# Optimization experiments

Measured on AMD Instinct MI355X. Metric: run time of the kernel, lower is better.

Reference implementation:

```python
import jax, jax.numpy as jnp
import numpy as np
from jax import lax

NUM_NODES = 100000
FEAT = 256
RANK = 16
NNZ = 4000000
NUM_HE = 125000  # num_hyperedges == num_edges_total
K = 2000000      # int(0.5 * NNZ)


def setup_inputs() -> dict:
    key = jax.random.key(0)
    ks = jax.random.split(key, 6)
    x = jax.random.normal(ks[0], (NUM_NODES, FEAT), dtype=jnp.float32)
    W = jax.random.normal(ks[1], (RANK, FEAT), dtype=jnp.float32)
    edge_factors = jax.random.normal(ks[2], (NUM_HE, RANK), dtype=jnp.float32)
    V_idx = jax.random.randint(ks[3], (NNZ,), 0, NUM_NODES, dtype=jnp.int32)
    E_idx = jax.random.randint(ks[4], (NNZ,), 0, NUM_HE, dtype=jnp.int32)
    edge_ids = jax.random.randint(ks[5], (NUM_HE,), 0, NUM_HE, dtype=jnp.int32)
    return {"x": x, "W": W, "edge_factors": edge_factors,
            "V_idx": V_idx, "E_idx": E_idx, "edge_ids": edge_ids, "k": K}


def _segment_mean(vals, seg_ids, num_segments):
    s = jax.ops.segment_sum(vals, seg_ids, num_segments=num_segments)
    c = jax.ops.segment_sum(jnp.ones_like(vals), seg_ids, num_segments=num_segments)
    return s / jnp.maximum(c, 1.0)


def reference(x, W, edge_factors, V_idx, E_idx, edge_ids, k):
    # node_proj(x): [N, rank]; gather per-incidence node and edge factors, dot product
    proj = x @ W.T                                  # [N, rank]
    ef = edge_factors[edge_ids[E_idx]]              # [nnz, rank]
    logits = jnp.sum(proj[V_idx] * ef, axis=-1)     # [nnz]
    scores = jax.nn.sigmoid(logits)

    # is_test=True path: deterministic top-k keep set
    _, keep_ids = lax.top_k(scores, k)
    hard = jnp.zeros_like(scores).at[keep_ids].set(1.0)
    # straight-through: forward == hard, gradient flows through scores where hard==1
    soft = hard + (scores - lax.stop_gradient(scores)) * hard

    edge_probs = _segment_mean(lax.stop_gradient(scores), E_idx, NUM_HE)
    edge_soft = _segment_mean(soft, E_idx, NUM_HE)
    edge_hard = (_segment_mean(hard, E_idx, NUM_HE) > 0).astype(jnp.float32)
    return scores, soft, hard, edge_probs, edge_soft, edge_hard
```

## Files before the change

kernel.cpp:

```cpp
#include <hip/hip_runtime.h>
#include <math.h>

#define FEAT 256
#define RANKK 16
#define CAND_CAP 131072
#define TIE_CAP 2048
#define NBK_MAX 512
#define PB_CHUNK 8192
#define SPLIT 4
#define PRJ_NODES 64
#define EH_BLOCKS 128
#define NW_BLOCKS 1024

typedef unsigned long long u64;

static __device__ __forceinline__ u64 pack_pair(unsigned e_low, unsigned bits, unsigned idx) {
    return ((u64)e_low << 56) | ((u64)bits << 26) | (u64)idx;
}
static __device__ __forceinline__ u64 pack_v(unsigned v, unsigned idx, unsigned e_low) {
    return ((u64)v << 40) | ((u64)idx << 8) | (u64)e_low;
}

__global__ __launch_bounds__(256) void prep_all(
        const int* __restrict__ E_idx, unsigned* __restrict__ bucketCnt,
        unsigned* __restrict__ bucketBase, unsigned* __restrict__ cursor,
        unsigned* __restrict__ ticket, int nnz,
        const float4* __restrict__ ef, const int* __restrict__ edge_ids,
        float4* __restrict__ ef2, int nhe,
        const float* __restrict__ x, const float* __restrict__ Wm,
        float* __restrict__ proj, int n_nodes, int G) {
    __shared__ float smem[12608];
    __shared__ unsigned isLast;
    int t = threadIdx.x;
    int bid = blockIdx.x;

    if (bid < EH_BLOCKS) {
        unsigned* h  = (unsigned*)smem;
        unsigned* ps = ((unsigned*)smem) + 512;
        for (int j = t; j < NBK_MAX; j += 256) h[j] = 0;
        __syncthreads();
        for (int i = bid * 256 + t; i < nnz; i += EH_BLOCKS * 256)
            atomicAdd(&h[((unsigned)E_idx[i]) >> 8], 1u);
        __syncthreads();
        for (int j = t; j < NBK_MAX; j += 256)
            if (h[j]) atomicAdd(&bucketCnt[j], h[j]);
        __threadfence();
        if (t == 0) isLast = (atomicAdd(ticket, 1u) == EH_BLOCKS - 1) ? 1u : 0u;
        __syncthreads();
        if (!isLast) return;
        unsigned a0 = atomicAdd(&bucketCnt[2 * t], 0u);
        unsigned a1 = atomicAdd(&bucketCnt[2 * t + 1], 0u);
        unsigned pairsum = a0 + a1;
        ps[t] = pairsum;
        __syncthreads();
        for (int off = 1; off < 256; off <<= 1) {
            unsigned v = (t >= off) ? ps[t - off] : 0u;
            __syncthreads();
            ps[t] += v;
            __syncthreads();
        }
        unsigned excl = ps[t] - pairsum;
        bucketBase[2 * t] = excl;           cursor[2 * t] = excl;
        bucketBase[2 * t + 1] = excl + a0;  cursor[2 * t + 1] = excl + a0;
        if (t == 255) bucketBase[NBK_MAX] = ps[255];
        return;
    }
    if (bid < EH_BLOCKS + G) {
        int tt = (bid - EH_BLOCKS) * 256 + t;
        if (tt < nhe * 4) {
            int e = tt >> 2, c = tt & 3;
            ef2[(size_t)e * 4 + c] = ef[(size_t)edge_ids[e] * 4 + c];
        }
        return;
    }
    int pb = bid - EH_BLOCKS - G;
    float (*Ws)[FEAT + 4] = (float(*)[FEAT + 4])smem;
    float (*Xs)[128 + 4]  = (float(*)[128 + 4])(smem + 4160);
    const float4* x4 = (const float4*)x;
    const float4* w4 = (const float4*)Wm;
    for (int i = t; i < RANKK * 64; i += 256) {
        int r = i >> 6, c4 = i & 63;
        *(float4*)&Ws[r][c4 * 4] = w4[(size_t)r * 64 + c4];
    }
    int nodeBase = pb * PRJ_NODES;
    int np = t >> 3, rp = t & 7;
    int n0 = np * 2, r0 = rp * 2;
    double a00 = 0.0, a01 = 0.0, a10 = 0.0, a11 = 0.0;
    for (int chunk = 0; chunk < 2; ++chunk) {
        __syncthreads();
        for (int i = t; i < PRJ_NODES * 32; i += 256) {
            int row = i >> 5, c4 = i & 31;
            int node = nodeBase + row;
            float4 v = make_float4(0.f, 0.f, 0.f, 0.f);
            if (node < n_nodes) v = x4[(size_t)node * 64 + chunk * 32 + c4];
            *(float4*)&Xs[row][c4 * 4] = v;
        }
        __syncthreads();
        int jw = chunk * 128;
        #pragma unroll 8
        for (int j4 = 0; j4 < 32; ++j4) {
            float4 xa = *(const float4*)&Xs[n0][j4 * 4];
            float4 xb = *(const float4*)&Xs[n0 + 1][j4 * 4];
            float4 wa = *(const float4*)&Ws[r0][jw + j4 * 4];
            float4 wb = *(const float4*)&Ws[r0 + 1][jw + j4 * 4];
            a00 += (double)xa.x * wa.x + (double)xa.y * wa.y + (double)xa.z * wa.z + (double)xa.w * wa.w;
            a01 += (double)xa.x * wb.x + (double)xa.y * wb.y + (double)xa.z * wb.z + (double)xa.w * wb.w;
            a10 += (double)xb.x * wa.x + (double)xb.y * wa.y + (double)xb.z * wa.z + (double)xb.w * wa.w;
            a11 += (double)xb.x * wb.x + (double)xb.y * wb.y + (double)xb.z * wb.z + (double)xb.w * wb.w;
        }
    }
    int nodeA = nodeBase + n0;
    int nodeB = nodeA + 1;
    if (nodeA < n_nodes) {
        proj[(size_t)nodeA * RANKK + r0]     = (float)a00;
        proj[(size_t)nodeA * RANKK + r0 + 1] = (float)a01;
    }
    if (nodeB < n_nodes) {
        proj[(size_t)nodeB * RANKK + r0]     = (float)a10;
        proj[(size_t)nodeB * RANKK + r0 + 1] = (float)a11;
    }
}

__global__ __launch_bounds__(256) void sort_kernel(const int* __restrict__ V_idx,
        const int* __restrict__ E_idx, u64* __restrict__ vlist,
        unsigned* __restrict__ cursor, int nnz, int nb) {
    __shared__ unsigned bh[NBK_MAX];
    int t = threadIdx.x;
    for (int j = t; j < NBK_MAX; j += 256) bh[j] = 0;
    __syncthreads();
    int base = blockIdx.x * PB_CHUNK;
    int nE = nnz - base;
    if (nE > PB_CHUNK) nE = PB_CHUNK;
    for (int o = t; o < nE; o += 256)
        atomicAdd(&bh[((unsigned)E_idx[base + o]) >> 8], 1u);
    __syncthreads();
    for (int b = t; b < nb; b += 256) {
        unsigned c = bh[b];
        bh[b] = c ? atomicAdd(&cursor[b], c) : 0u;
    }
    __syncthreads();
    for (int o = t; o < nE; o += 256) {
        int i = base + o;
        unsigned e = (unsigned)E_idx[i];
        unsigned v = (unsigned)V_idx[i];
        unsigned pos = atomicAdd(&bh[e >> 8], 1u);
        vlist[pos] = pack_v(v, (unsigned)i, e & 255u);
    }
}

__global__ __launch_bounds__(256) void bucket_score(
        const float4* __restrict__ proj4, const float4* __restrict__ ef4,
        const unsigned* __restrict__ bucketBase, u64* __restrict__ list,
        float* __restrict__ scores, int nhe) {
    __shared__ float efs[256][20];
    int t = threadIdx.x;
    int b = blockIdx.x >> 2;
    int part = blockIdx.x & (SPLIT - 1);
    for (int jj = t; jj < 1024; jj += 256) {
        int edge = (b << 8) + (jj >> 2);
        if (edge < nhe) {
            float4 v = ef4[(size_t)edge * 4 + (jj & 3)];
            *(float4*)&efs[jj >> 2][(jj & 3) * 4] = v;
        }
    }
    __syncthreads();
    unsigned n0 = bucketBase[b], n1 = bucketBase[b + 1];
    #pragma unroll 2
    for (unsigned j = n0 + (part << 8) + t; j < n1; j += SPLIT * 256) {
        u64 p = list[j];
        unsigned v   = (unsigned)(p >> 40);
        unsigned idx = (unsigned)(p >> 8) & 0xFFFFFFu;
        unsigned el  = (unsigned)(p & 255u);
        float4 p0 = proj4[(size_t)v * 4 + 0];
        float4 p1 = proj4[(size_t)v * 4 + 1];
        float4 p2 = proj4[(size_t)v * 4 + 2];
        float4 p3 = proj4[(size_t)v * 4 + 3];
        float4 f0 = *(const float4*)&efs[el][0];
        float4 f1 = *(const float4*)&efs[el][4];
        float4 f2 = *(const float4*)&efs[el][8];
        float4 f3 = *(const float4*)&efs[el][12];
        double acc = (double)p0.x * f0.x + (double)p0.y * f0.y + (double)p0.z * f0.z + (double)p0.w * f0.w
                   + (double)p1.x * f1.x + (double)p1.y * f1.y + (double)p1.z * f1.z + (double)p1.w * f1.w
                   + (double)p2.x * f2.x + (double)p2.y * f2.y + (double)p2.z * f2.z + (double)p2.w * f2.w
                   + (double)p3.x * f3.x + (double)p3.y * f3.y + (double)p3.z * f3.z + (double)p3.w * f3.w;
        float s = (float)(1.0 / (1.0 + exp(-acc)));
        scores[idx] = s;
        list[j] = pack_pair(el, __float_as_uint(s), idx);
    }
}

__global__ __launch_bounds__(256) void score_linear(
        const float4* __restrict__ proj4, const float4* __restrict__ ef4,
        const int* __restrict__ V_idx, const int* __restrict__ E_idx,
        float* __restrict__ scores, int nnz) {
    int stride = gridDim.x * blockDim.x;
    #pragma unroll 2
    for (int i = blockIdx.x * blockDim.x + threadIdx.x; i < nnz; i += stride) {
        int v = V_idx[i], e = E_idx[i];
        float4 p0 = proj4[(size_t)v * 4 + 0];
        float4 p1 = proj4[(size_t)v * 4 + 1];
        float4 p2 = proj4[(size_t)v * 4 + 2];
        float4 p3 = proj4[(size_t)v * 4 + 3];
        float4 f0 = ef4[(size_t)e * 4 + 0];
        float4 f1 = ef4[(size_t)e * 4 + 1];
        float4 f2 = ef4[(size_t)e * 4 + 2];
        float4 f3 = ef4[(size_t)e * 4 + 3];
        double acc = (double)p0.x * f0.x + (double)p0.y * f0.y + (double)p0.z * f0.z + (double)p0.w * f0.w
                   + (double)p1.x * f1.x + (double)p1.y * f1.y + (double)p1.z * f1.z + (double)p1.w * f1.w
                   + (double)p2.x * f2.x + (double)p2.y * f2.y + (double)p2.z * f2.z + (double)p2.w * f2.w
                   + (double)p3.x * f3.x + (double)p3.y * f3.y + (double)p3.z * f3.z + (double)p3.w * f3.w;
        scores[i] = (float)(1.0 / (1.0 + exp(-acc)));
    }
}
__global__ __launch_bounds__(256) void pair_build(const int* __restrict__ E_idx,
        const float* __restrict__ scores, u64* __restrict__ pairs,
        unsigned* __restrict__ cursor, int nnz, int nb) {
    __shared__ unsigned bh[NBK_MAX];
    for (int t = threadIdx.x; t < NBK_MAX; t += 256) bh[t] = 0;
    __syncthreads();
    int base = blockIdx.x * PB_CHUNK;
    int nE = nnz - base;
    if (nE > PB_CHUNK) nE = PB_CHUNK;
    for (int o = threadIdx.x; o < nE; o += 256)
        atomicAdd(&bh[((unsigned)E_idx[base + o]) >> 8], 1u);
    __syncthreads();
    for (int b = threadIdx.x; b < nb; b += 256) {
        unsigned c = bh[b];
        bh[b] = c ? atomicAdd(&cursor[b], c) : 0u;
    }
    __syncthreads();
    for (int o = threadIdx.x; o < nE; o += 256) {
        int i = base + o;
        unsigned e = (unsigned)E_idx[i];
        unsigned bits = __float_as_uint(scores[i]);
        unsigned pos = atomicAdd(&bh[e >> 8], 1u);
        pairs[pos] = pack_pair(e & 255u, bits, (unsigned)i);
    }
}

__global__ __launch_bounds__(256) void hist1scan(const float4* __restrict__ scores4,
        unsigned* __restrict__ hist1g, unsigned* __restrict__ ticket,
        unsigned* __restrict__ sel, const int* __restrict__ kptr, int n4, int nnz) {
    __shared__ unsigned h[4096];
    __shared__ unsigned sfx[256];
    __shared__ unsigned isLast;
    int t = threadIdx.x;
    for (int j = t; j < 4096; j += 256) h[j] = 0;
    __syncthreads();
    unsigned r1016 = 0, r1015 = 0, r0 = 0;
    int stride = gridDim.x * 256;
    for (int i = blockIdx.x * 256 + t; i < n4; i += stride) {
        float4 sv = scores4[i];
        unsigned bb[4] = {__float_as_uint(sv.x), __float_as_uint(sv.y),
                          __float_as_uint(sv.z), __float_as_uint(sv.w)};
        #pragma unroll
        for (int q = 0; q < 4; ++q) {
            unsigned b = bb[q] >> 20;
            if (b == 1016) ++r1016;
            else if (b == 1015) ++r1015;
            else if (b == 0) ++r0;
            else atomicAdd(&h[b], 1u);
        }
    }
    for (int i = n4 * 4 + blockIdx.x * 256 + t; i < nnz; i += stride) {
        unsigned b = __float_as_uint(((const float*)scores4)[i]) >> 20;
        if (b == 1016) ++r1016;
        else if (b == 1015) ++r1015;
        else if (b == 0) ++r0;
        else atomicAdd(&h[b], 1u);
    }
    if (r1016) atomicAdd(&h[1016], r1016);
    if (r1015) atomicAdd(&h[1015], r1015);
    if (r0) atomicAdd(&h[0], r0);
    __syncthreads();
    for (int j = t; j < 4096; j += 256)
        if (h[j]) atomicAdd(&hist1g[j], h[j]);
    __threadfence();
    if (t == 0) isLast = (atomicAdd(ticket, 1u) == gridDim.x - 1) ? 1u : 0u;
    __syncthreads();
    if (!isLast) return;
    unsigned local[16];
    unsigned s = 0;
    #pragma unroll
    for (int j = 0; j < 16; ++j) { local[j] = atomicAdd(&hist1g[t * 16 + j], 0u); s += local[j]; }
    sfx[t] = s;
    __syncthreads();
    for (int off = 1; off < 256; off <<= 1) {
        unsigned add = (t + off < 256) ? sfx[t + off] : 0;
        __syncthreads();
        sfx[t] += add;
        __syncthreads();
    }
    unsigned krem = (unsigned)(*kptr);
    unsigned above = (t + 1 < 256) ? sfx[t + 1] : 0;
    if (above < krem && sfx[t] >= krem) {
        unsigned cum = above;
        int b = t * 16;
        for (int j = 15; j >= 0; --j) {
            unsigned cc = local[j];
            if (cum + cc >= krem) { b = t * 16 + j; break; }
            cum += cc;
        }
        sel[0] = krem - cum;
        sel[1] = ((unsigned)b) << 20;
    }
}

__global__ void compact_kernel(const float4* __restrict__ scores4,
                               const unsigned* __restrict__ sel,
                               uint2* __restrict__ cand, unsigned* __restrict__ candCount,
                               int n4, int nnz) {
    unsigned pref = sel[1] >> 20;
    int tid = blockIdx.x * blockDim.x + threadIdx.x;
    int stride = gridDim.x * blockDim.x;
    int lane = threadIdx.x & 63;
    int niter = (n4 + stride - 1) / stride;
    for (int kk = 0; kk < niter; ++kk) {
        int i = tid + kk * stride;
        bool inb = (i < n4);
        float4 sv = make_float4(0.f, 0.f, 0.f, 0.f);
        if (inb) sv = scores4[i];
        unsigned bb[4] = {__float_as_uint(sv.x), __float_as_uint(sv.y),
                          __float_as_uint(sv.z), __float_as_uint(sv.w)};
        #pragma unroll
        for (int q = 0; q < 4; ++q) {
            bool pred = inb && ((bb[q] >> 20) == pref);
            unsigned long long mask = __ballot(pred);
            if (mask) {
                int leader = __ffsll(mask) - 1;
                unsigned base = 0;
                if (lane == leader) base = atomicAdd(candCount, (unsigned)__popcll(mask));
                base = __shfl(base, leader, 64);
                if (pred) {
                    unsigned rank = __popcll(mask & ((1ull << lane) - 1ull));
                    unsigned pos = base + rank;
                    if (pos < CAND_CAP) cand[pos] = make_uint2(bb[q], (unsigned)(i * 4 + q));
                }
            }
        }
    }
    for (int i = n4 * 4 + tid; i < nnz; i += stride) {
        unsigned b = __float_as_uint(((const float*)scores4)[i]);
        if ((b >> 20) == pref) {
            unsigned pos = atomicAdd(candCount, 1u);
            if (pos < CAND_CAP) cand[pos] = make_uint2(b, (unsigned)i);
        }
    }
}

__global__ __launch_bounds__(256) void select_small(const uint2* __restrict__ cand,
                            const unsigned* __restrict__ candCount,
                            unsigned* __restrict__ sel, unsigned* __restrict__ tieList) {
    __shared__ unsigned h2[4096];
    __shared__ unsigned sfx[256];
    __shared__ unsigned sB2, sKrem2, sT, sM;
    __shared__ unsigned h3[256];
    __shared__ unsigned ties[TIE_CAP];
    __shared__ unsigned tcnt;
    int t = threadIdx.x;
    unsigned nc = *candCount;
    int n = (nc < CAND_CAP) ? (int)nc : CAND_CAP;
    unsigned krem = sel[0];
    unsigned pref = sel[1];

    for (int j = t; j < 4096; j += 256) h2[j] = 0;
    if (t == 0) tcnt = 0;
    __syncthreads();
    for (int j = t; j < n; j += 256) atomicAdd(&h2[(cand[j].x >> 8) & 0xFFF], 1u);
    __syncthreads();

    unsigned local[16];
    unsigned s = 0;
    #pragma unroll
    for (int j = 0; j < 16; ++j) { local[j] = h2[t * 16 + j]; s += local[j]; }
    sfx[t] = s;
    __syncthreads();
    for (int off = 1; off < 256; off <<= 1) {
        unsigned add = (t + off < 256) ? sfx[t + off] : 0;
        __syncthreads();
        sfx[t] += add;
        __syncthreads();
    }
    {
        unsigned above = (t + 1 < 256) ? sfx[t + 1] : 0;
        if (above < krem && sfx[t] >= krem) {
            unsigned cum = above;
            int b = t * 16;
            for (int j = 15; j >= 0; --j) {
                unsigned cc = local[j];
                if (cum + cc >= krem) { b = t * 16 + j; break; }
                cum += cc;
            }
            sB2 = (unsigned)b;
            sKrem2 = krem - cum;
        }
    }
    __syncthreads();

    h3[t] = 0;
    __syncthreads();
    unsigned b2 = sB2;
    for (int j = t; j < n; j += 256) {
        unsigned x = cand[j].x;
        if (((x >> 8) & 0xFFF) == b2) atomicAdd(&h3[x & 0xFF], 1u);
    }
    __syncthreads();
    sfx[t] = h3[t];
    __syncthreads();
    for (int off = 1; off < 256; off <<= 1) {
        unsigned add = (t + off < 256) ? sfx[t + off] : 0;
        __syncthreads();
        sfx[t] += add;
        __syncthreads();
    }
    {
        unsigned krem2 = sKrem2;
        unsigned above = (t + 1 < 256) ? sfx[t + 1] : 0;
        if (above < krem2 && sfx[t] >= krem2) {
            sT = pref | (b2 << 8) | (unsigned)t;
            sM = krem2 - above;
        }
    }
    __syncthreads();

    unsigned T = sT;
    for (int j = t; j < n; j += 256) {
        if (cand[j].x == T) {
            unsigned p = atomicAdd(&tcnt, 1u);
            if (p < TIE_CAP) ties[p] = cand[j].y;
        }
    }
    __syncthreads();
    if (t == 0) {
        unsigned cnt = (tcnt < TIE_CAP) ? tcnt : TIE_CAP;
        for (unsigned a = 1; a < cnt; ++a) {
            unsigned key = ties[a];
            int bpos = (int)a - 1;
            while (bpos >= 0 && ties[bpos] > key) { ties[bpos + 1] = ties[bpos]; --bpos; }
            ties[bpos + 1] = key;
        }
        unsigned m = sM;
        if (m > cnt) m = cnt;
        sel[2] = T;
        sel[3] = m;
        for (unsigned j = 0; j < m; ++j) tieList[j] = ties[j];
    }
}

__global__ __launch_bounds__(256) void final_combo(const u64* __restrict__ pairs,
        const unsigned* __restrict__ bucketBase, const unsigned* __restrict__ sel,
        const unsigned* __restrict__ tieList, const float4* __restrict__ scores4,
        float* __restrict__ eprob, float* __restrict__ esoft, float* __restrict__ ehard,
        float4* __restrict__ hard4, float4* __restrict__ soft4,
        int nb, int n4, int nnz, int nhe) {
    __shared__ float ss[256];
    __shared__ unsigned cc[256];
    __shared__ unsigned hh[256];
    __shared__ unsigned ties[TIE_CAP];
    unsigned T = sel[2];
    unsigned m = sel[3];
    if (m > TIE_CAP) m = TIE_CAP;
    int t = threadIdx.x;
    for (int j = t; j < (int)m; j += 256) ties[j] = tieList[j];

    if ((int)blockIdx.x < nb) {
        ss[t] = 0.f; cc[t] = 0u; hh[t] = 0u;
        __syncthreads();
        int b = blockIdx.x;
        unsigned n0 = bucketBase[b], n1 = bucketBase[b + 1];
        for (unsigned j = n0 + t; j < n1; j += 256) {
            u64 p = pairs[j];
            unsigned el = (unsigned)(p >> 56);
            unsigned bits = (unsigned)(p >> 26) & 0x3FFFFFFFu;
            atomicAdd(&ss[el], __uint_as_float(bits));
            atomicAdd(&cc[el], 1u);
            bool keep = bits > T;
            if (bits == T) {
                unsigned idx = (unsigned)(p & 0x3FFFFFFu);
                int lo = 0, hi = (int)m - 1;
                keep = false;
                while (lo <= hi) {
                    int mid = (lo + hi) >> 1;
                    unsigned v = ties[mid];
                    if (v == idx) { keep = true; break; }
                    if (v < idx) lo = mid + 1; else hi = mid - 1;
                }
            }
            if (keep) atomicAdd(&hh[el], 1u);
        }
        __syncthreads();
        int e = blockIdx.x * 256 + t;
        if (e < nhe) {
            float c = fmaxf((float)cc[t], 1.0f);
            eprob[e] = ss[t] / c;
            esoft[e] = (float)hh[t] / c;
            ehard[e] = (hh[t] > 0) ? 1.0f : 0.0f;
        }
        return;
    }
    __syncthreads();
    int tid = (blockIdx.x - nb) * 256 + t;
    int stride = NW_BLOCKS * 256;
    for (int i = tid; i < n4; i += stride) {
        float4 sv = scores4[i];
        unsigned bb[4] = {__float_as_uint(sv.x), __float_as_uint(sv.y),
                          __float_as_uint(sv.z), __float_as_uint(sv.w)};
        float hv[4];
        #pragma unroll
        for (int q = 0; q < 4; ++q) {
            bool keep = (bb[q] > T);
            if (bb[q] == T) {
                unsigned idx = (unsigned)(i * 4 + q);
                int lo = 0, hi = (int)m - 1;
                keep = false;
                while (lo <= hi) {
                    int mid = (lo + hi) >> 1;
                    unsigned v = ties[mid];
                    if (v == idx) { keep = true; break; }
                    if (v < idx) lo = mid + 1; else hi = mid - 1;
                }
            }
            hv[q] = keep ? 1.0f : 0.0f;
        }
        float4 outv = make_float4(hv[0], hv[1], hv[2], hv[3]);
        hard4[i] = outv;
        soft4[i] = outv;
    }
    const float* sc = (const float*)scores4;
    float* hard = (float*)hard4;
    float* soft = (float*)soft4;
    for (int i = n4 * 4 + tid; i < nnz; i += stride) {
        unsigned b = __float_as_uint(sc[i]);
        bool keep = (b > T);
        if (b == T) {
            unsigned idx = (unsigned)i;
            int lo = 0, hi = (int)m - 1;
            keep = false;
            while (lo <= hi) {
                int mid = (lo + hi) >> 1;
                unsigned v = ties[mid];
                if (v == idx) { keep = true; break; }
                if (v < idx) lo = mid + 1; else hi = mid - 1;
            }
        }
        float hvv = keep ? 1.0f : 0.0f;
        hard[i] = hvv;
        soft[i] = hvv;
    }
}

__global__ __launch_bounds__(256) void edge_final(const u64* __restrict__ pairs,
        const unsigned* __restrict__ bucketBase, const unsigned* __restrict__ sel,
        const unsigned* __restrict__ tieList,
        float* __restrict__ eprob, float* __restrict__ esoft, float* __restrict__ ehard,
        int nhe) {
    __shared__ float ss[256];
    __shared__ unsigned cc[256];
    __shared__ unsigned hh[256];
    __shared__ unsigned ties[TIE_CAP];
    unsigned T = sel[2];
    unsigned m = sel[3];
    if (m > TIE_CAP) m = TIE_CAP;
    int t = threadIdx.x;
    ss[t] = 0.f; cc[t] = 0u; hh[t] = 0u;
    for (int j = t; j < (int)m; j += 256) ties[j] = tieList[j];
    __syncthreads();
    int b = blockIdx.x;
    unsigned n0 = bucketBase[b], n1 = bucketBase[b + 1];
    for (unsigned j = n0 + t; j < n1; j += 256) {
        u64 p = pairs[j];
        unsigned el = (unsigned)(p >> 56);
        unsigned bits = (unsigned)(p >> 26) & 0x3FFFFFFFu;
        atomicAdd(&ss[el], __uint_as_float(bits));
        atomicAdd(&cc[el], 1u);
        bool keep = bits > T;
        if (bits == T) {
            unsigned idx = (unsigned)(p & 0x3FFFFFFu);
            int lo = 0, hi = (int)m - 1;
            keep = false;
            while (lo <= hi) {
                int mid = (lo + hi) >> 1;
                unsigned v = ties[mid];
                if (v == idx) { keep = true; break; }
                if (v < idx) lo = mid + 1; else hi = mid - 1;
            }
        }
        if (keep) atomicAdd(&hh[el], 1u);
    }
    __syncthreads();
    int e = b * 256 + t;
    if (e < nhe) {
        float c = fmaxf((float)cc[t], 1.0f);
        eprob[e] = ss[t] / c;
        esoft[e] = (float)hh[t] / c;
        ehard[e] = (hh[t] > 0) ? 1.0f : 0.0f;
    }
}
__global__ __launch_bounds__(256) void write_hard(const float4* __restrict__ scores4,
                           const unsigned* __restrict__ sel,
                           const unsigned* __restrict__ tieList,
                           float4* __restrict__ hard4, float4* __restrict__ soft4,
                           int n4, int nnz) {
    __shared__ unsigned ties[TIE_CAP];
    unsigned T = sel[2];
    unsigned m = sel[3];
    if (m > TIE_CAP) m = TIE_CAP;
    for (int j = threadIdx.x; j < (int)m; j += blockDim.x) ties[j] = tieList[j];
    __syncthreads();
    int tid = blockIdx.x * blockDim.x + threadIdx.x;
    int stride = gridDim.x * blockDim.x;
    for (int i = tid; i < n4; i += stride) {
        float4 sv = scores4[i];
        unsigned bb[4] = {__float_as_uint(sv.x), __float_as_uint(sv.y),
                          __float_as_uint(sv.z), __float_as_uint(sv.w)};
        float hv[4];
        #pragma unroll
        for (int q = 0; q < 4; ++q) {
            bool keep = (bb[q] > T);
            if (bb[q] == T) {
                unsigned idx = (unsigned)(i * 4 + q);
                int lo = 0, hi = (int)m - 1;
                keep = false;
                while (lo <= hi) {
                    int mid = (lo + hi) >> 1;
                    unsigned v = ties[mid];
                    if (v == idx) { keep = true; break; }
                    if (v < idx) lo = mid + 1; else hi = mid - 1;
                }
            }
            hv[q] = keep ? 1.0f : 0.0f;
        }
        float4 outv = make_float4(hv[0], hv[1], hv[2], hv[3]);
        hard4[i] = outv;
        soft4[i] = outv;
    }
    const float* sc = (const float*)scores4;
    float* hard = (float*)hard4;
    float* soft = (float*)soft4;
    for (int i = n4 * 4 + tid; i < nnz; i += stride) {
        unsigned b = __float_as_uint(sc[i]);
        bool keep = (b > T);
        if (b == T) {
            unsigned idx = (unsigned)i;
            int lo = 0, hi = (int)m - 1;
            keep = false;
            while (lo <= hi) {
                int mid = (lo + hi) >> 1;
                unsigned v = ties[mid];
                if (v == idx) { keep = true; break; }
                if (v < idx) lo = mid + 1; else hi = mid - 1;
            }
        }
        float hvv = keep ? 1.0f : 0.0f;
        hard[i] = hvv;
        soft[i] = hvv;
    }
}

extern "C" void kernel_launch(void* const* d_in, const int* in_sizes, int n_in,
                              void* d_out, int out_size, void* d_ws, size_t ws_size,
                              hipStream_t stream) {
    const float* x        = (const float*)d_in[0];
    const float* Wm       = (const float*)d_in[1];
    const float* ef       = (const float*)d_in[2];
    const int*   V_idx    = (const int*)d_in[3];
    const int*   E_idx    = (const int*)d_in[4];
    const int*   edge_ids = (const int*)d_in[5];
    const int*   kptr     = (const int*)d_in[6];

    const int nnz     = in_sizes[3];
    const int nhe     = in_sizes[5];
    const int n_nodes = in_sizes[0] / FEAT;
    const int nb      = (nhe + 255) >> 8;

    float* out    = (float*)d_out;
    float* scores = out;
    float* soft   = out + (size_t)nnz;
    float* hard   = out + 2 * (size_t)nnz;
    float* eprob  = out + 3 * (size_t)nnz;
    float* esoft  = eprob + nhe;
    float* ehard  = esoft + nhe;

    uint2* cand = (uint2*)eprob;

    char* w = (char*)d_ws;
    unsigned* hist1      = (unsigned*)w;
    unsigned* bucketCnt  = hist1 + 4096;
    unsigned* candCount  = bucketCnt + NBK_MAX;
    unsigned* ticket1    = candCount + 1;
    unsigned* ticket2    = ticket1 + 1;
    unsigned* sel        = ticket2 + 1;
    unsigned* tieList    = sel + 8;
    unsigned* bucketBase = tieList + TIE_CAP;
    unsigned* cursor     = bucketBase + NBK_MAX + 1;
    char* auxEnd = (char*)(cursor + NBK_MAX);
    size_t auxAligned = (((size_t)(auxEnd - w)) + 255) & ~(size_t)255;
    size_t zeroBytes = (size_t)(4096 + NBK_MAX + 3) * sizeof(unsigned);

    size_t ef2Bytes   = (size_t)nhe * RANKK * sizeof(float);
    size_t projBytes  = (size_t)n_nodes * RANKK * sizeof(float);
    size_t pairsBytes = (size_t)nnz * sizeof(u64);

    bool wsBig  = (ws_size >= auxAligned + ef2Bytes + projBytes);
    bool wsHuge = (ws_size >= auxAligned + ef2Bytes + projBytes + pairsBytes);

    float* ef2;
    float* proj;
    u64*   vlist;
    if (wsBig) {
        ef2  = (float*)(w + auxAligned);
        proj = (float*)(w + auxAligned + ef2Bytes);
        vlist = wsHuge ? (u64*)(w + auxAligned + ef2Bytes + projBytes) : (u64*)soft;
    } else {
        ef2  = hard;
        proj = hard + (size_t)nhe * RANKK;
        vlist = (u64*)soft;
    }

    hipMemsetAsync(w, 0, zeroBytes, stream);

    int G = (nhe * 4 + 255) / 256;
    int P = (n_nodes + PRJ_NODES - 1) / PRJ_NODES;
    prep_all<<<EH_BLOCKS + G + P, 256, 0, stream>>>(
        E_idx, bucketCnt, bucketBase, cursor, ticket1, nnz,
        (const float4*)ef, edge_ids, (float4*)ef2, nhe,
        x, Wm, proj, n_nodes, G);

    int nChunks = (nnz + PB_CHUNK - 1) / PB_CHUNK;
    if (wsBig) {
        sort_kernel<<<nChunks, 256, 0, stream>>>(V_idx, E_idx, vlist, cursor, nnz, nb);
        bucket_score<<<nb * SPLIT, 256, 0, stream>>>(
            (const float4*)proj, (const float4*)ef2, bucketBase, vlist, scores, nhe);
    } else {
        score_linear<<<2048, 256, 0, stream>>>(
            (const float4*)proj, (const float4*)ef2, V_idx, E_idx, scores, nnz);
        pair_build<<<nChunks, 256, 0, stream>>>(E_idx, scores, vlist, cursor, nnz, nb);
    }

    int n4 = nnz / 4;
    hist1scan<<<128, 256, 0, stream>>>((const float4*)scores, hist1, ticket2,
                                       sel, kptr, n4, nnz);
    compact_kernel<<<1024, 256, 0, stream>>>(
        (const float4*)scores, sel, cand, candCount, n4, nnz);
    select_small<<<1, 256, 0, stream>>>(cand, candCount, sel, tieList);

    if (wsHuge) {
        final_combo<<<nb + NW_BLOCKS, 256, 0, stream>>>(
            vlist, bucketBase, sel, tieList, (const float4*)scores,
            eprob, esoft, ehard, (float4*)hard, (float4*)soft, nb, n4, nnz, nhe);
    } else {
        edge_final<<<nb, 256, 0, stream>>>(vlist, bucketBase, sel, tieList,
                                           eprob, esoft, ehard, nhe);
        write_hard<<<1024, 256, 0, stream>>>(
            (const float4*)scores, sel, tieList, (float4*)hard, (float4*)soft, n4, nnz);
    }
}
```

Measured before the change: 444.8 us.

## Fuse top-k histogram, compaction and selection into one persistent kernel

```diff
diff --git a/kernel.cpp b/kernel.cpp
--- a/kernel.cpp
+++ b/kernel.cpp
@@ -11,6 +11,8 @@
 #define PRJ_NODES 64
 #define EH_BLOCKS 128
 #define NW_BLOCKS 1024
+#define TK_BLOCKS 1024
+#define NK 4
 
 typedef unsigned long long u64;
 
@@ -238,6 +240,233 @@
     }
 }
 
+__global__ __launch_bounds__(256, 4) void topk_fused(
+        const float4* __restrict__ scores4,
+        unsigned* __restrict__ hist1g, unsigned* __restrict__ ticketA,
+        unsigned* __restrict__ flagSel, unsigned* __restrict__ ticketB,
+        unsigned* __restrict__ sel, const int* __restrict__ kptr,
+        uint2* __restrict__ cand, unsigned* __restrict__ candCount,
+        unsigned* __restrict__ tieList, int n4, int nnz) {
+    __shared__ unsigned h[4096];
+    __shared__ unsigned sfx[256];
+    __shared__ unsigned h3[256];
+    __shared__ unsigned ties[TIE_CAP];
+    __shared__ unsigned sB2, sKrem2, sT, sM, tcnt, isLast;
+    int t = threadIdx.x;
+    int bid = blockIdx.x;
+    int lane = t & 63;
+
+    for (int j = t; j < 4096; j += 256) h[j] = 0;
+    __syncthreads();
+    float4 sv[NK];
+    bool have[NK];
+    unsigned r1016 = 0, r1015 = 0, r0 = 0;
+    #pragma unroll
+    for (int k = 0; k < NK; ++k) {
+        int i = bid * 256 + t + k * (TK_BLOCKS * 256);
+        have[k] = (i < n4);
+        sv[k] = make_float4(0.f, 0.f, 0.f, 0.f);
+        if (have[k]) sv[k] = scores4[i];
+        if (have[k]) {
+            unsigned bb[4] = {__float_as_uint(sv[k].x), __float_as_uint(sv[k].y),
+                              __float_as_uint(sv[k].z), __float_as_uint(sv[k].w)};
+            #pragma unroll
+            for (int q = 0; q < 4; ++q) {
+                unsigned b = bb[q] >> 20;
+                if (b == 1016) ++r1016;
+                else if (b == 1015) ++r1015;
+                else if (b == 0) ++r0;
+                else atomicAdd(&h[b], 1u);
+            }
+        }
+    }
+    float stail = 0.f;
+    bool haveTail = false;
+    {
+        int tpos = bid * 256 + t;
+        int ntail = nnz - n4 * 4;
+        if (tpos < ntail) {
+            haveTail = true;
+            stail = ((const float*)scores4)[n4 * 4 + tpos];
+            unsigned b = __float_as_uint(stail) >> 20;
+            if (b == 1016) ++r1016;
+            else if (b == 1015) ++r1015;
+            else if (b == 0) ++r0;
+            else atomicAdd(&h[b], 1u);
+        }
+    }
+    if (r1016) atomicAdd(&h[1016], r1016);
+    if (r1015) atomicAdd(&h[1015], r1015);
+    if (r0) atomicAdd(&h[0], r0);
+    __syncthreads();
+    for (int j = t; j < 4096; j += 256)
+        if (h[j]) atomicAdd(&hist1g[j], h[j]);
+    __threadfence();
+    if (t == 0) isLast = (atomicAdd(ticketA, 1u) == TK_BLOCKS - 1) ? 1u : 0u;
+    __syncthreads();
+
+    if (isLast) {
+        unsigned local[16];
+        unsigned s = 0;
+        #pragma unroll
+        for (int j = 0; j < 16; ++j) { local[j] = atomicAdd(&hist1g[t * 16 + j], 0u); s += local[j]; }
+        sfx[t] = s;
+        __syncthreads();
+        for (int off = 1; off < 256; off <<= 1) {
+            unsigned add = (t + off < 256) ? sfx[t + off] : 0;
+            __syncthreads();
+            sfx[t] += add;
+            __syncthreads();
+        }
+        unsigned krem = (unsigned)(*kptr);
+        unsigned above = (t + 1 < 256) ? sfx[t + 1] : 0;
+        if (above < krem && sfx[t] >= krem) {
+            unsigned cum = above;
+            int b = t * 16;
+            for (int j = 15; j >= 0; --j) {
+                unsigned cc = local[j];
+                if (cum + cc >= krem) { b = t * 16 + j; break; }
+                cum += cc;
+            }
+            sel[0] = krem - cum;
+            sel[1] = ((unsigned)b) << 20;
+        }
+        __syncthreads();
+        __threadfence();
+        if (t == 0) atomicExch(flagSel, 1u);
+    } else {
+        if (t == 0) { while (atomicAdd(flagSel, 0u) == 0u) { } }
+        __syncthreads();
+    }
+    unsigned pref = atomicAdd(&sel[1], 0u) >> 20;
+
+    #pragma unroll
+    for (int k = 0; k < NK; ++k) {
+        int i = bid * 256 + t + k * (TK_BLOCKS * 256);
+        unsigned bb[4] = {__float_as_uint(sv[k].x), __float_as_uint(sv[k].y),
+                          __float_as_uint(sv[k].z), __float_as_uint(sv[k].w)};
+        #pragma unroll
+        for (int q = 0; q < 4; ++q) {
+            bool pred = have[k] && ((bb[q] >> 20) == pref);
+            unsigned long long mask = __ballot(pred);
+            if (mask) {
+                int leader = __ffsll(mask) - 1;
+                unsigned base = 0;
+                if (lane == leader) base = atomicAdd(candCount, (unsigned)__popcll(mask));
+                base = __shfl(base, leader, 64);
+                if (pred) {
+                    unsigned rank = __popcll(mask & ((1ull << lane) - 1ull));
+                    unsigned pos = base + rank;
+                    if (pos < CAND_CAP) cand[pos] = make_uint2(bb[q], (unsigned)(i * 4 + q));
+                }
+            }
+        }
+    }
+    if (haveTail) {
+        unsigned b = __float_as_uint(stail);
+        if ((b >> 20) == pref) {
+            unsigned pos = atomicAdd(candCount, 1u);
+            if (pos < CAND_CAP) cand[pos] = make_uint2(b, (unsigned)(n4 * 4 + bid * 256 + t));
+        }
+    }
+    __threadfence();
+    if (t == 0) isLast = (atomicAdd(ticketB, 1u) == TK_BLOCKS - 1) ? 1u : 0u;
+    __syncthreads();
+    if (!isLast) return;
+
+    volatile const uint2* vcand = (volatile const uint2*)cand;
+    unsigned nc = atomicAdd(candCount, 0u);
+    int n = (nc < CAND_CAP) ? (int)nc : CAND_CAP;
+    unsigned krem = atomicAdd(&sel[0], 0u);
+    unsigned prefbits = atomicAdd(&sel[1], 0u);
+
+    for (int j = t; j < 4096; j += 256) h[j] = 0;
+    if (t == 0) tcnt = 0;
+    __syncthreads();
+    for (int j = t; j < n; j += 256) atomicAdd(&h[(vcand[j].x >> 8) & 0xFFF], 1u);
+    __syncthreads();
+
+    unsigned local[16];
+    unsigned s = 0;
+    #pragma unroll
+    for (int j = 0; j < 16; ++j) { local[j] = h[t * 16 + j]; s += local[j]; }
+    sfx[t] = s;
+    __syncthreads();
+    for (int off = 1; off < 256; off <<= 1) {
+        unsigned add = (t + off < 256) ? sfx[t + off] : 0;
+        __syncthreads();
+        sfx[t] += add;
+        __syncthreads();
+    }
+    {
+        unsigned above = (t + 1 < 256) ? sfx[t + 1] : 0;
+        if (above < krem && sfx[t] >= krem) {
+            unsigned cum = above;
+            int b = t * 16;
+            for (int j = 15; j >= 0; --j) {
+                unsigned cc = local[j];
+                if (cum + cc >= krem) { b = t * 16 + j; break; }
+                cum += cc;
+            }
+            sB2 = (unsigned)b;
+            sKrem2 = krem - cum;
+        }
+    }
+    __syncthreads();
+
+    h3[t] = 0;
+    __syncthreads();
+    unsigned b2 = sB2;
+    for (int j = t; j < n; j += 256) {
+        unsigned xx = vcand[j].x;
+        if (((xx >> 8) & 0xFFF) == b2) atomicAdd(&h3[xx & 0xFF], 1u);
+    }
+    __syncthreads();
+    sfx[t] = h3[t];
+    __syncthreads();
+    for (int off = 1; off < 256; off <<= 1) {
+        unsigned add = (t + off < 256) ? sfx[t + off] : 0;
+        __syncthreads();
+        sfx[t] += add;
+        __syncthreads();
+    }
+    {
+        unsigned krem2 = sKrem2;
+        unsigned above = (t + 1 < 256) ? sfx[t + 1] : 0;
+        if (above < krem2 && sfx[t] >= krem2) {
+            sT = prefbits | (b2 << 8) | (unsigned)t;
+            sM = krem2 - above;
+        }
+    }
+    __syncthreads();
+
+    unsigned T = sT;
+    for (int j = t; j < n; j += 256) {
+        uint2 cj;
+        cj.x = vcand[j].x;
+        cj.y = vcand[j].y;
+        if (cj.x == T) {
+            unsigned p = atomicAdd(&tcnt, 1u);
+            if (p < TIE_CAP) ties[p] = cj.y;
+        }
+    }
+    __syncthreads();
+    if (t == 0) {
+        unsigned cnt = (tcnt < TIE_CAP) ? tcnt : TIE_CAP;
+        for (unsigned a = 1; a < cnt; ++a) {
+            unsigned key = ties[a];
+            int bpos = (int)a - 1;
+            while (bpos >= 0 && ties[bpos] > key) { ties[bpos + 1] = ties[bpos]; --bpos; }
+            ties[bpos + 1] = key;
+        }
+        unsigned m = sM;
+        if (m > cnt) m = cnt;
+        sel[2] = T;
+        sel[3] = m;
+        for (unsigned j = 0; j < m; ++j) tieList[j] = ties[j];
+    }
+}
+
 __global__ __launch_bounds__(256) void hist1scan(const float4* __restrict__ scores4,
         unsigned* __restrict__ hist1g, unsigned* __restrict__ ticket,
         unsigned* __restrict__ sel, const int* __restrict__ kptr, int n4, int nnz) {
@@ -305,7 +534,6 @@
         sel[1] = ((unsigned)b) << 20;
     }
 }
-
 __global__ void compact_kernel(const float4* __restrict__ scores4,
                                const unsigned* __restrict__ sel,
                                uint2* __restrict__ cand, unsigned* __restrict__ candCount,
@@ -347,7 +575,6 @@
         }
     }
 }
-
 __global__ __launch_bounds__(256) void select_small(const uint2* __restrict__ cand,
                             const unsigned* __restrict__ candCount,
                             unsigned* __restrict__ sel, unsigned* __restrict__ tieList) {
@@ -362,13 +589,11 @@
     int n = (nc < CAND_CAP) ? (int)nc : CAND_CAP;
     unsigned krem = sel[0];
     unsigned pref = sel[1];
-
     for (int j = t; j < 4096; j += 256) h2[j] = 0;
     if (t == 0) tcnt = 0;
     __syncthreads();
     for (int j = t; j < n; j += 256) atomicAdd(&h2[(cand[j].x >> 8) & 0xFFF], 1u);
     __syncthreads();
-
     unsigned local[16];
     unsigned s = 0;
     #pragma unroll
@@ -396,7 +621,6 @@
         }
     }
     __syncthreads();
-
     h3[t] = 0;
     __syncthreads();
     unsigned b2 = sB2;
@@ -422,7 +646,6 @@
         }
     }
     __syncthreads();
-
     unsigned T = sT;
     for (int j = t; j < n; j += 256) {
         if (cand[j].x == T) {
@@ -688,14 +911,16 @@
     unsigned* bucketCnt  = hist1 + 4096;
     unsigned* candCount  = bucketCnt + NBK_MAX;
     unsigned* ticket1    = candCount + 1;
-    unsigned* ticket2    = ticket1 + 1;
-    unsigned* sel        = ticket2 + 1;
+    unsigned* ticketA    = ticket1 + 1;
+    unsigned* ticketB    = ticketA + 1;
+    unsigned* flagSel    = ticketB + 1;
+    unsigned* sel        = flagSel + 1;
     unsigned* tieList    = sel + 8;
     unsigned* bucketBase = tieList + TIE_CAP;
     unsigned* cursor     = bucketBase + NBK_MAX + 1;
     char* auxEnd = (char*)(cursor + NBK_MAX);
     size_t auxAligned = (((size_t)(auxEnd - w)) + 255) & ~(size_t)255;
-    size_t zeroBytes = (size_t)(4096 + NBK_MAX + 3) * sizeof(unsigned);
+    size_t zeroBytes = (size_t)(4096 + NBK_MAX + 5) * sizeof(unsigned);
 
     size_t ef2Bytes   = (size_t)nhe * RANKK * sizeof(float);
     size_t projBytes  = (size_t)n_nodes * RANKK * sizeof(float);
@@ -738,11 +963,17 @@
     }
 
     int n4 = nnz / 4;
-    hist1scan<<<128, 256, 0, stream>>>((const float4*)scores, hist1, ticket2,
-                                       sel, kptr, n4, nnz);
-    compact_kernel<<<1024, 256, 0, stream>>>(
-        (const float4*)scores, sel, cand, candCount, n4, nnz);
-    select_small<<<1, 256, 0, stream>>>(cand, candCount, sel, tieList);
+    if (n4 <= NK * TK_BLOCKS * 256 && nnz - n4 * 4 <= TK_BLOCKS * 256) {
+        topk_fused<<<TK_BLOCKS, 256, 0, stream>>>(
+            (const float4*)scores, hist1, ticketA, flagSel, ticketB,
+            sel, kptr, cand, candCount, tieList, n4, nnz);
+    } else {
+        hist1scan<<<128, 256, 0, stream>>>((const float4*)scores, hist1, ticketA,
+                                           sel, kptr, n4, nnz);
+        compact_kernel<<<1024, 256, 0, stream>>>(
+            (const float4*)scores, sel, cand, candCount, n4, nnz);
+        select_small<<<1, 256, 0, stream>>>(cand, candCount, sel, tieList);
+    }
 
     if (wsHuge) {
         final_combo<<<nb + NW_BLOCKS, 256, 0, stream>>>(
```

Result: slower. 536.9 us (+20.7%).
